# Optimization experiments

Measured on AMD Instinct MI355X. Metric: run time of the kernel, lower is better.

Reference implementation:

```python
import jax, jax.numpy as jnp
import numpy as np

H = 512   # hidden_dim
B = 1024  # batch
D = 256   # history length


def setup_inputs() -> dict:
    key = jax.random.key(0)
    k1, k2, k3, k4, k5, k6 = jax.random.split(key, 6)
    return {
        "h_tilde": jax.random.normal(k1, (B, H), dtype=jnp.float32),
        "c_t": jax.random.normal(k2, (B, H), dtype=jnp.float32),
        "h_history": jax.random.normal(k3, (B, D, H), dtype=jnp.float32),
        # learned parameters (nn.Linear stores weight as [out, in]; y = x @ W.T)
        "Waq": jax.random.normal(k4, (H, 2 * H), dtype=jnp.float32) * (1.0 / np.sqrt(2 * H)),
        "Wah": jax.random.normal(k5, (H, H), dtype=jnp.float32) * (1.0 / np.sqrt(H)),
        "ba": jnp.zeros((H,), dtype=jnp.float32),
        "v_t": jax.random.normal(k6, (H,), dtype=jnp.float32),
    }


def reference(h_tilde, c_t, h_history, Waq, Wah, ba, v_t):
    # q_t = [h_tilde ; c_t] -> [B, 2H]; project to [B, H]
    q_t = jnp.concatenate([h_tilde, c_t], axis=1)
    q_proj = q_t @ Waq.T                         # [B, H]
    h_proj = jnp.einsum('bdh,gh->bdg', h_history, Wah)  # [B, D, H]
    # broadcast add + tanh: the large [B, D, H] intermediate
    score_pre = jnp.tanh(q_proj[:, None, :] + h_proj + ba)
    alpha_unscaled = jnp.einsum('bdh,h->bd', score_pre, v_t)  # [B, D]
    alpha = jax.nn.softmax(alpha_unscaled, axis=1)            # [B, D]
    e_t = jnp.einsum('bd,bdh->bh', alpha, h_history)          # [B, H]
    return (e_t, alpha)
```

## Files before the change

kernel.cpp:

```cpp
#include <hip/hip_runtime.h>
#include <hip/hip_bf16.h>

#define HDIM 512
#define BDIM 1024
#define DDIM 256
#define MTOT (BDIM * DDIM)

typedef _Float16 half8 __attribute__((ext_vector_type(8)));
typedef float f32x4 __attribute__((ext_vector_type(4)));

__device__ __forceinline__ float ftanh(float x) {
    float e = __expf(2.0f * x);
    float d = e + 1.0f;
    float r;
    asm("v_rcp_f32 %0, %1" : "=v"(r) : "v"(d));
    return 1.0f - 2.0f * r;
}

__device__ __forceinline__ void gl_lds16(const _Float16* src, _Float16* dst) {
    __builtin_amdgcn_global_load_lds((const __attribute__((address_space(1))) void*)src,
                                     (__attribute__((address_space(3))) void*)dst,
                                     16, 0, 0);
}

__global__ __launch_bounds__(256) void k_prep(const float* __restrict__ h_tilde,
                                              const float* __restrict__ c_t,
                                              const float* __restrict__ Waq,
                                              const float* __restrict__ ba,
                                              const float* __restrict__ Wah,
                                              float* __restrict__ qb,
                                              _Float16* __restrict__ W16) {
    __shared__ float qs[4][1024];
    int t = threadIdx.x;
    if (blockIdx.x >= 256) {
        int n = (blockIdx.x - 256) * 256 + t;
        int chunk = n >> 10, r = n & 1023;
        int kb = r >> 6, kp = (r >> 4) & 3, g = r & 15;
        const float* src = Wah + (size_t)(chunk * 16 + g) * 512 + kb * 32 + kp * 8;
        float4 v0 = *(const float4*)src;
        float4 v1 = *(const float4*)(src + 4);
        half8 h;
        h[0] = (_Float16)v0.x; h[1] = (_Float16)v0.y; h[2] = (_Float16)v0.z; h[3] = (_Float16)v0.w;
        h[4] = (_Float16)v1.x; h[5] = (_Float16)v1.y; h[6] = (_Float16)v1.z; h[7] = (_Float16)v1.w;
        *(half8*)&W16[(size_t)n * 8] = h;
        return;
    }
    int b0 = blockIdx.x * 4;
    #pragma unroll
    for (int p = 0; p < 4; p++) {
        int f4 = t + p * 256;
        int e = f4 * 4;
        int row = e >> 10, k = e & 1023;
        float4 v;
        if (k < 512) v = *(const float4*)&h_tilde[(b0 + row) * 512 + k];
        else         v = *(const float4*)&c_t[(b0 + row) * 512 + k - 512];
        *(float4*)&qs[row][k] = v;
    }
    __syncthreads();
    int g0 = t, g1 = t + 256;
    float acc0[4] = {0.f, 0.f, 0.f, 0.f};
    float acc1[4] = {0.f, 0.f, 0.f, 0.f};
    const float4* w0p = (const float4*)&Waq[(size_t)g0 * 1024];
    const float4* w1p = (const float4*)&Waq[(size_t)g1 * 1024];
    #pragma unroll 4
    for (int k4 = 0; k4 < 256; k4++) {
        float4 w0 = w0p[k4];
        float4 w1 = w1p[k4];
        #pragma unroll
        for (int bb = 0; bb < 4; bb++) {
            float4 q = *(const float4*)&qs[bb][k4 * 4];
            acc0[bb] += q.x * w0.x + q.y * w0.y + q.z * w0.z + q.w * w0.w;
            acc1[bb] += q.x * w1.x + q.y * w1.y + q.z * w1.z + q.w * w1.w;
        }
    }
    #pragma unroll
    for (int bb = 0; bb < 4; bb++) {
        qb[(b0 + bb) * 512 + g0] = acc0[bb] + ba[g0];
        qb[(b0 + bb) * 512 + g1] = acc1[bb] + ba[g1];
    }
}

__global__ __launch_bounds__(256, 4) void k_logits(const float* __restrict__ hist,
                                                   const float* __restrict__ qb,
                                                   const _Float16* __restrict__ W16,
                                                   const float* __restrict__ v_t,
                                                   float* __restrict__ logits,
                                                   float* __restrict__ eparts,
                                                   float* __restrict__ ms) {
    __shared__ _Float16 Wb[2][8192];
    __shared__ float qbs[512];
    __shared__ float vsh[512];
    __shared__ float lsh[64];

    int t = threadIdx.x;
    int w = t >> 6, lane = t & 63, l15 = lane & 15, l4 = lane >> 4;
    int bx = blockIdx.x;
    size_t m_base = (size_t)bx * 64;
    int b = bx >> 2;
    int off = ((bx >> 3) & 3) * 8;

    qbs[t] = qb[b * 512 + t];
    qbs[t + 256] = qb[b * 512 + 256 + t];
    vsh[t] = v_t[t];
    vsh[t + 256] = v_t[256 + t];

    #pragma unroll
    for (int sg = 0; sg < 4; sg++)
        gl_lds16(W16 + (size_t)off * 8192 + ((size_t)(w * 4 + sg) * 64 + lane) * 8,
                 &Wb[0][(w * 4 + sg) * 512]);

    half8 afr[16];
    const float* xb = hist + (m_base + w * 16 + l15) * 512 + l4 * 8;
    {
        float4 xr0[4], xr1[4];
        #pragma unroll
        for (int u = 0; u < 4; u++) {
            xr0[u] = *(const float4*)(xb + u * 32);
            xr1[u] = *(const float4*)(xb + u * 32 + 4);
        }
        #pragma unroll
        for (int kb = 0; kb < 16; kb++) {
            const int slot = kb & 3;
            float4 v0 = xr0[slot];
            float4 v1 = xr1[slot];
            if (kb + 4 < 16) {
                xr0[slot] = *(const float4*)(xb + (kb + 4) * 32);
                xr1[slot] = *(const float4*)(xb + (kb + 4) * 32 + 4);
            }
            half8 h;
            h[0] = (_Float16)v0.x; h[1] = (_Float16)v0.y; h[2] = (_Float16)v0.z; h[3] = (_Float16)v0.w;
            h[4] = (_Float16)v1.x; h[5] = (_Float16)v1.y; h[6] = (_Float16)v1.z; h[7] = (_Float16)v1.w;
            afr[kb] = h;
        }
    }

    float S[4] = {0.f, 0.f, 0.f, 0.f};

    __syncthreads();

    const _Float16* bufbase0 = &Wb[0][lane * 8];
    const _Float16* bufbase1 = &Wb[1][lane * 8];

    for (int c = 0; c < 32; c++) {
        int cc = (c + off) & 31;
        int cur = c & 1;
        if (c < 31) {
            int cn = (cc + 1) & 31;
            const _Float16* wc = W16 + (size_t)cn * 8192;
            _Float16* wd = Wb[cur ^ 1];
            #pragma unroll
            for (int sg = 0; sg < 4; sg++)
                gl_lds16(wc + ((size_t)(w * 4 + sg) * 64 + lane) * 8,
                         &wd[(w * 4 + sg) * 512]);
        }
        float qv = qbs[cc * 16 + l15];
        float vv = vsh[cc * 16 + l15];
        const _Float16* bufp = cur ? bufbase1 : bufbase0;
        f32x4 tac = (f32x4){0.f, 0.f, 0.f, 0.f};
        __builtin_amdgcn_s_setprio(1);
        #pragma unroll
        for (int kb = 0; kb < 16; kb++) {
            half8 bf = *(const half8*)(bufp + kb * 512);
            tac = __builtin_amdgcn_mfma_f32_16x16x32_f16(afr[kb], bf, tac, 0, 0, 0);
        }
        __builtin_amdgcn_s_setprio(0);
        #pragma unroll
        for (int j = 0; j < 4; j++)
            S[j] += ftanh(tac[j] + qv) * vv;
        __syncthreads();
    }

    #pragma unroll
    for (int j = 0; j < 4; j++) {
        float s = S[j];
        s += __shfl_xor(s, 1, 64);
        s += __shfl_xor(s, 2, 64);
        s += __shfl_xor(s, 4, 64);
        s += __shfl_xor(s, 8, 64);
        if (l15 == 0) {
            logits[m_base + w * 16 + l4 * 4 + j] = s;
            lsh[w * 16 + l4 * 4 + j] = s;
        }
    }
    __syncthreads();

    float lv = lsh[lane];
    float mb = lv;
    mb = fmaxf(mb, __shfl_xor(mb, 1, 64));
    mb = fmaxf(mb, __shfl_xor(mb, 2, 64));
    mb = fmaxf(mb, __shfl_xor(mb, 4, 64));
    mb = fmaxf(mb, __shfl_xor(mb, 8, 64));
    mb = fmaxf(mb, __shfl_xor(mb, 16, 64));
    mb = fmaxf(mb, __shfl_xor(mb, 32, 64));
    float eb = __expf(lv - mb);
    float sb = eb;
    sb += __shfl_xor(sb, 1, 64);
    sb += __shfl_xor(sb, 2, 64);
    sb += __shfl_xor(sb, 4, 64);
    sb += __shfl_xor(sb, 8, 64);
    sb += __shfl_xor(sb, 16, 64);
    sb += __shfl_xor(sb, 32, 64);

    float coef = __expf(lsh[w * 16 + l15] - mb);
    float* ews = (float*)Wb;
    #pragma unroll
    for (int kb = 0; kb < 16; kb++) {
        float ep[8];
        half8 x = afr[kb];
        #pragma unroll
        for (int e2 = 0; e2 < 8; e2++) ep[e2] = coef * (float)x[e2];
        #pragma unroll
        for (int e2 = 0; e2 < 8; e2++) {
            ep[e2] += __shfl_xor(ep[e2], 1, 64);
            ep[e2] += __shfl_xor(ep[e2], 2, 64);
            ep[e2] += __shfl_xor(ep[e2], 4, 64);
            ep[e2] += __shfl_xor(ep[e2], 8, 64);
        }
        if (l15 == 0) {
            #pragma unroll
            for (int e2 = 0; e2 < 8; e2++)
                ews[w * 512 + kb * 32 + l4 * 8 + e2] = ep[e2];
        }
    }
    __syncthreads();
    float v0 = ews[t] + ews[512 + t] + ews[1024 + t] + ews[1536 + t];
    float v1 = ews[256 + t] + ews[768 + t] + ews[1280 + t] + ews[1792 + t];
    eparts[(size_t)bx * 512 + t] = v0;
    eparts[(size_t)bx * 512 + 256 + t] = v1;
    if (t == 0) { ms[bx * 2] = mb; ms[bx * 2 + 1] = sb; }
}

__global__ __launch_bounds__(256) void k_comb(const float* __restrict__ logits,
                                              const float* __restrict__ eparts,
                                              const float* __restrict__ ms,
                                              float* __restrict__ out) {
    int b = blockIdx.x, t = threadIdx.x;
    float m0 = ms[(4 * b + 0) * 2], s0 = ms[(4 * b + 0) * 2 + 1];
    float m1 = ms[(4 * b + 1) * 2], s1 = ms[(4 * b + 1) * 2 + 1];
    float m2 = ms[(4 * b + 2) * 2], s2 = ms[(4 * b + 2) * 2 + 1];
    float m3 = ms[(4 * b + 3) * 2], s3 = ms[(4 * b + 3) * 2 + 1];
    float m = fmaxf(fmaxf(m0, m1), fmaxf(m2, m3));
    float w0 = __expf(m0 - m), w1 = __expf(m1 - m);
    float w2 = __expf(m2 - m), w3 = __expf(m3 - m);
    float Sb = w0 * s0 + w1 * s1 + w2 * s2 + w3 * s3;
    float l = logits[b * 256 + t];
    out[BDIM * HDIM + b * 256 + t] = __expf(l - m) / Sb;
    const float* ep = eparts + (size_t)(4 * b) * 512;
    float a0 = w0 * ep[t] + w1 * ep[512 + t] + w2 * ep[1024 + t] + w3 * ep[1536 + t];
    float a1 = w0 * ep[256 + t] + w1 * ep[768 + t] + w2 * ep[1280 + t] + w3 * ep[1792 + t];
    out[b * 512 + t] = a0 / Sb;
    out[b * 512 + 256 + t] = a1 / Sb;
}

extern "C" void kernel_launch(void* const* d_in, const int* in_sizes, int n_in,
                              void* d_out, int out_size, void* d_ws, size_t ws_size,
                              hipStream_t stream) {
    const float* h_tilde = (const float*)d_in[0];
    const float* c_t     = (const float*)d_in[1];
    const float* hist    = (const float*)d_in[2];
    const float* Waq     = (const float*)d_in[3];
    const float* Wah     = (const float*)d_in[4];
    const float* ba      = (const float*)d_in[5];
    const float* v_t     = (const float*)d_in[6];
    float* out = (float*)d_out;

    char* ws = (char*)d_ws;
    float*    qb     = (float*)ws;
    _Float16* W16    = (_Float16*)(ws + (2u << 20));
    float*    logits = (float*)(ws + (3u << 20));
    float*    eparts = (float*)(ws + (4u << 20));
    float*    ms     = (float*)(ws + (12u << 20));

    k_prep<<<384, 256, 0, stream>>>(h_tilde, c_t, Waq, ba, Wah, qb, W16);
    k_logits<<<4096, 256, 0, stream>>>(hist, qb, W16, v_t, logits, eparts, ms);
    k_comb<<<1024, 256, 0, stream>>>(logits, eparts, ms, out);
}
```

Before: 382.9 us.

## Triple-buffer half-chunk weight tiles with vmcnt waits and retile q projection

The logits kernel now streams the fp16 weight in 64 half-chunks (8 k-blocks each) through a three-slot LDS ring. It waits on an explicit vmcnt count plus a single barrier per phase instead of double-buffered full chunks with a trailing __syncthreads. This keeps two loads in flight and replaces the syncthreads drain, at the cost of more barriers and hand-written waitcnt assumptions. The prep kernel also regroups the q projection so each block handles 16 batch rows by 128 outputs, reusing each weight load across 8 rows, and the W16 layout is changed to match the half-chunk order.

Result: slower. 1.190 ms (+210.7%).

```diff
diff --git a/kernel.cpp b/kernel.cpp
--- a/kernel.cpp
+++ b/kernel.cpp
@@ -30,13 +30,14 @@
                                               const float* __restrict__ Wah,
                                               float* __restrict__ qb,
                                               _Float16* __restrict__ W16) {
-    __shared__ float qs[4][1024];
+    __shared__ float qs[16][1024];
     int t = threadIdx.x;
     if (blockIdx.x >= 256) {
         int n = (blockIdx.x - 256) * 256 + t;
-        int chunk = n >> 10, r = n & 1023;
+        int p = n >> 9, r = n & 511;
         int kb = r >> 6, kp = (r >> 4) & 3, g = r & 15;
-        const float* src = Wah + (size_t)(chunk * 16 + g) * 512 + kb * 32 + kp * 8;
+        int c = p >> 1, kh = p & 1;
+        const float* src = Wah + (size_t)(c * 16 + g) * 512 + kh * 256 + kb * 32 + kp * 8;
         float4 v0 = *(const float4*)src;
         float4 v1 = *(const float4*)(src + 4);
         half8 h;
@@ -45,39 +46,35 @@
         *(half8*)&W16[(size_t)n * 8] = h;
         return;
     }
-    int b0 = blockIdx.x * 4;
-    #pragma unroll
-    for (int p = 0; p < 4; p++) {
-        int f4 = t + p * 256;
-        int e = f4 * 4;
-        int row = e >> 10, k = e & 1023;
+    int bt = blockIdx.x >> 2, gq = blockIdx.x & 3;
+    int b0 = bt * 16;
+    #pragma unroll
+    for (int i = 0; i < 16; i++) {
+        int idx = t + i * 256;
+        int row = idx >> 8, k = (idx & 255) * 4;
         float4 v;
         if (k < 512) v = *(const float4*)&h_tilde[(b0 + row) * 512 + k];
         else         v = *(const float4*)&c_t[(b0 + row) * 512 + k - 512];
         *(float4*)&qs[row][k] = v;
     }
     __syncthreads();
-    int g0 = t, g1 = t + 256;
-    float acc0[4] = {0.f, 0.f, 0.f, 0.f};
-    float acc1[4] = {0.f, 0.f, 0.f, 0.f};
-    const float4* w0p = (const float4*)&Waq[(size_t)g0 * 1024];
-    const float4* w1p = (const float4*)&Waq[(size_t)g1 * 1024];
-    #pragma unroll 4
+    int g = gq * 128 + (t & 127);
+    int bh = t >> 7;
+    float acc[8] = {0.f, 0.f, 0.f, 0.f, 0.f, 0.f, 0.f, 0.f};
+    const float4* wp = (const float4*)&Waq[(size_t)g * 1024];
+    #pragma unroll 2
     for (int k4 = 0; k4 < 256; k4++) {
-        float4 w0 = w0p[k4];
-        float4 w1 = w1p[k4];
-        #pragma unroll
-        for (int bb = 0; bb < 4; bb++) {
-            float4 q = *(const float4*)&qs[bb][k4 * 4];
-            acc0[bb] += q.x * w0.x + q.y * w0.y + q.z * w0.z + q.w * w0.w;
-            acc1[bb] += q.x * w1.x + q.y * w1.y + q.z * w1.z + q.w * w1.w;
-        }
-    }
-    #pragma unroll
-    for (int bb = 0; bb < 4; bb++) {
-        qb[(b0 + bb) * 512 + g0] = acc0[bb] + ba[g0];
-        qb[(b0 + bb) * 512 + g1] = acc1[bb] + ba[g1];
-    }
+        float4 wv = wp[k4];
+        #pragma unroll
+        for (int j = 0; j < 8; j++) {
+            float4 q = *(const float4*)&qs[bh * 8 + j][k4 * 4];
+            acc[j] += q.x * wv.x + q.y * wv.y + q.z * wv.z + q.w * wv.w;
+        }
+    }
+    float bav = ba[g];
+    #pragma unroll
+    for (int j = 0; j < 8; j++)
+        qb[(b0 + bh * 8 + j) * 512 + g] = acc[j] + bav;
 }
 
 __global__ __launch_bounds__(256, 4) void k_logits(const float* __restrict__ hist,
@@ -87,7 +84,7 @@
                                                    float* __restrict__ logits,
                                                    float* __restrict__ eparts,
                                                    float* __restrict__ ms) {
-    __shared__ _Float16 Wb[2][8192];
+    __shared__ _Float16 Wb[3][4096];
     __shared__ float qbs[512];
     __shared__ float vsh[512];
     __shared__ float lsh[64];
@@ -97,7 +94,7 @@
     int bx = blockIdx.x;
     size_t m_base = (size_t)bx * 64;
     int b = bx >> 2;
-    int off = ((bx >> 3) & 3) * 8;
+    int offp = ((bx >> 3) & 3) * 16;
 
     qbs[t] = qb[b * 512 + t];
     qbs[t + 256] = qb[b * 512 + 256 + t];
@@ -105,9 +102,13 @@
     vsh[t + 256] = v_t[256 + t];
 
     #pragma unroll
-    for (int sg = 0; sg < 4; sg++)
-        gl_lds16(W16 + (size_t)off * 8192 + ((size_t)(w * 4 + sg) * 64 + lane) * 8,
-                 &Wb[0][(w * 4 + sg) * 512]);
+    for (int pp = 0; pp < 2; pp++) {
+        const _Float16* wc = W16 + (size_t)((pp + offp) & 63) * 4096;
+        #pragma unroll
+        for (int sg = 0; sg < 2; sg++)
+            gl_lds16(wc + ((size_t)(w * 2 + sg) * 64 + lane) * 8,
+                     &Wb[pp][(w * 2 + sg) * 512]);
+    }
 
     half8 afr[16];
     const float* xb = hist + (m_base + w * 16 + l15) * 512 + l4 * 8;
@@ -135,40 +136,49 @@
     }
 
     float S[4] = {0.f, 0.f, 0.f, 0.f};
-
-    __syncthreads();
-
-    const _Float16* bufbase0 = &Wb[0][lane * 8];
-    const _Float16* bufbase1 = &Wb[1][lane * 8];
-
-    for (int c = 0; c < 32; c++) {
-        int cc = (c + off) & 31;
-        int cur = c & 1;
-        if (c < 31) {
-            int cn = (cc + 1) & 31;
-            const _Float16* wc = W16 + (size_t)cn * 8192;
-            _Float16* wd = Wb[cur ^ 1];
-            #pragma unroll
-            for (int sg = 0; sg < 4; sg++)
-                gl_lds16(wc + ((size_t)(w * 4 + sg) * 64 + lane) * 8,
-                         &wd[(w * 4 + sg) * 512]);
-        }
-        float qv = qbs[cc * 16 + l15];
-        float vv = vsh[cc * 16 + l15];
-        const _Float16* bufp = cur ? bufbase1 : bufbase0;
-        f32x4 tac = (f32x4){0.f, 0.f, 0.f, 0.f};
-        __builtin_amdgcn_s_setprio(1);
-        #pragma unroll
-        for (int kb = 0; kb < 16; kb++) {
-            half8 bf = *(const half8*)(bufp + kb * 512);
-            tac = __builtin_amdgcn_mfma_f32_16x16x32_f16(afr[kb], bf, tac, 0, 0, 0);
-        }
-        __builtin_amdgcn_s_setprio(0);
-        #pragma unroll
-        for (int j = 0; j < 4; j++)
-            S[j] += ftanh(tac[j] + qv) * vv;
-        __syncthreads();
-    }
+    f32x4 tac = (f32x4){0.f, 0.f, 0.f, 0.f};
+
+    asm volatile("s_waitcnt lgkmcnt(0)" ::: "memory");
+
+#define PHASE_BODY(P, VMS, ISSUE)                                              \
+    {                                                                          \
+        const int p_ = (P);                                                    \
+        asm volatile("s_waitcnt vmcnt(" VMS ")" ::: "memory");                 \
+        __builtin_amdgcn_s_barrier();                                          \
+        if (ISSUE) {                                                           \
+            const _Float16* wc_ = W16 + (size_t)((p_ + 2 + offp) & 63) * 4096; \
+            _Float16* wd_ = Wb[(p_ + 2) % 3];                                  \
+            _Pragma("unroll")                                                  \
+            for (int sg_ = 0; sg_ < 2; sg_++)                                  \
+                gl_lds16(wc_ + ((size_t)(w * 2 + sg_) * 64 + lane) * 8,        \
+                         &wd_[(w * 2 + sg_) * 512]);                           \
+        }                                                                      \
+        const int pp_ = (p_ + offp) & 63;                                      \
+        const int cc_ = pp_ >> 1, kh_ = pp_ & 1;                               \
+        const _Float16* bufp_ = &Wb[p_ % 3][lane * 8];                         \
+        if (kh_ == 0) tac = (f32x4){0.f, 0.f, 0.f, 0.f};                       \
+        __builtin_amdgcn_s_setprio(1);                                         \
+        _Pragma("unroll")                                                      \
+        for (int kb_ = 0; kb_ < 8; kb_++) {                                    \
+            half8 bf = *(const half8*)(bufp_ + kb_ * 512);                     \
+            tac = __builtin_amdgcn_mfma_f32_16x16x32_f16(afr[kh_ * 8 + kb_], bf, tac, 0, 0, 0); \
+        }                                                                      \
+        __builtin_amdgcn_s_setprio(0);                                         \
+        if (kh_ == 1) {                                                        \
+            float qv = qbs[cc_ * 16 + l15];                                    \
+            float vv = vsh[cc_ * 16 + l15];                                    \
+            _Pragma("unroll")                                                  \
+            for (int j_ = 0; j_ < 4; j_++)                                     \
+                S[j_] += ftanh(tac[j_] + qv) * vv;                             \
+        }                                                                      \
+    }
+
+    for (int p = 0; p < 62; p++) {
+        PHASE_BODY(p, "2", true)
+    }
+    PHASE_BODY(62, "2", false)
+    PHASE_BODY(63, "0", false)
+#undef PHASE_BODY
 
     #pragma unroll
     for (int j = 0; j < 4; j++) {
```
